# Kernel tuning notes

Hardware: AMD Instinct MI355X
Metric: run time of the kernel (lower is better)

## Reference

```python
import jax, jax.numpy as jnp
import numpy as np

DEGREE = 64
LEN_H = 2
INIT_H = 4.0
FEATURES = [256, 512, 512, 256]
BATCH = 1024


def _frozen_kh():
    # get_frozen_para: k = arange(-floor(d/2), ceil(d/2)+1); h = 1/(init_h*(1+arange(len_h))) (inverse decay)
    k = jnp.arange(-np.floor(DEGREE / 2), np.ceil(DEGREE / 2) + 1, dtype=jnp.float32)  # (degree+1,)
    h = 1.0 / (INIT_H * (1.0 + jnp.arange(LEN_H, dtype=jnp.float32)))  # (len_h,)
    return k, h


def setup_inputs() -> dict:
    key = jax.random.key(0)
    ks = jax.random.split(key, 7)
    inp = {"x": jax.random.normal(ks[0], (BATCH, FEATURES[0]), dtype=jnp.float32)}
    i = 1
    for li, (fi, fo) in enumerate(zip(FEATURES[:-1], FEATURES[1:])):
        # initialization='None': plain normal coeffs (matches source)
        inp[f"coeffs{li}"] = jax.random.normal(ks[i], (fi, fo, LEN_H, DEGREE + 1), dtype=jnp.float32)
        inp[f"alpha{li}"] = jax.random.normal(ks[i + 1], (fi, fo), dtype=jnp.float32) / jnp.sqrt((fi + fo) / 2.0)
        inp[f"beta{li}"] = jnp.zeros((fo,), dtype=jnp.float32)
        i += 2
    return inp


def _sinc_layer(x, coeffs, alpha, beta, k, h):
    # x: (b, i); coeffs: (i, o, k_h, d+1); alpha: (i, o); beta: (o,)
    y_eqt = x @ alpha + beta  # skip connection (skip_mode=1)
    xa = jnp.tanh(x)  # activation='tanh'
    # tile across (len_h, degree+1), scale by 1/h, shift by k, then sinc
    xe = xa[:, :, None, None] / h[None, None, :, None] + k[None, None, None, :]  # (b, i, k_h, d+1)
    y = jnp.einsum("bikd,iokd->bo", jnp.sinc(xe), coeffs)
    return y_eqt + y


def reference(x, coeffs0, alpha0, beta0, coeffs1, alpha1, beta1, coeffs2, alpha2, beta2):
    k, h = _frozen_kh()
    x = jnp.tanh(x)  # normalizer
    for c, a, b in ((coeffs0, alpha0, beta0), (coeffs1, alpha1, beta1), (coeffs2, alpha2, beta2)):
        x = _sinc_layer(x, c, a, b, k, h)
    return x
```

## Files before the change

kernel.cpp:

```cpp
#include <hip/hip_runtime.h>
#include <hip/hip_bf16.h>
#include <cstdint>


#define PI_F 3.14159265358979323846f

typedef float floatx4 __attribute__((ext_vector_type(4)));
typedef __bf16 bf16x8 __attribute__((ext_vector_type(8)));

#define GLOAD_LDS16(gp, lp)                                                    \
  __builtin_amdgcn_global_load_lds(                                            \
      (const __attribute__((address_space(1))) void*)(uintptr_t)(const void*)(gp), \
      (__attribute__((address_space(3))) void*)(uint32_t)(uintptr_t)(void*)(lp),   \
      16, 0, 0)

static __device__ __forceinline__ void repack_body(
    const float* __restrict__ coeffs, const float* __restrict__ alpha,
    ushort* __restrict__ Bhi, ushort* __restrict__ Blo,
    int fo, int Kaug, int writeLo, int idx, int tid)
{
  int nchunksK = Kaug >> 8;
  int o     = idx / nchunksK;
  int chunk = idx - o * nchunksK;
  int r = chunk * 256 + tid;
  int i = r / 131;
  int j = r - i * 131;
  float v;
  if (j == 130) {
    v = alpha[(size_t)i * fo + o];
  } else {
    int h1 = (j >= 65) ? 1 : 0;
    int d  = j - (h1 ? 65 : 0);
    v = coeffs[(((size_t)i * fo + o) * 2 + h1) * 65 + d];
  }
  __hip_bfloat16 hb = __float2bfloat16(v);
  Bhi[(size_t)o * Kaug + r] = *(ushort*)&hb;
  if (writeLo) {
    __hip_bfloat16 lb = __float2bfloat16(v - __bfloat162float(hb));
    Blo[(size_t)o * Kaug + r] = *(ushort*)&lb;
  }
}

__global__ __launch_bounds__(256) void repack_all(
    const float* c0, const float* a0, ushort* h0, ushort* l0,
    const float* c1, const float* a1, ushort* h1, ushort* l1,
    const float* c2, const float* a2, ushort* h2,
    int fo0, int fo1, int fo2, int K0, int K1, int K2, int nb0, int nb01)
{
  int b = blockIdx.x, tid = threadIdx.x;
  if (b < nb0)        repack_body(c0, a0, h0, l0, fo0, K0, 1, b,        tid);
  else if (b < nb01)  repack_body(c1, a1, h1, l1, fo1, K1, 1, b - nb0,  tid);
  else                repack_body(c2, a2, h2, 0,  fo2, K2, 0, b - nb01, tid);
}

__global__ __launch_bounds__(256) void repack_kernel(
    const float* __restrict__ coeffs, const float* __restrict__ alpha,
    ushort* __restrict__ Bhi, ushort* __restrict__ Blo,
    int fo, int Kaug, int writeLo)
{
  repack_body(coeffs, alpha, Bhi, Blo, fo, Kaug, writeLo,
              blockIdx.x + blockIdx.y * gridDim.x, threadIdx.x);
}

__global__ __launch_bounds__(256) void act_kernel(
    const float* __restrict__ Xin, __hip_bfloat16* __restrict__ Ahi,
    __hip_bfloat16* __restrict__ Alo, int first, int writeLo)
{
  __shared__ float sm[256][5];
  int tid = threadIdx.x;
  int p0  = blockIdx.x * 256;
  {
    float x  = Xin[p0 + tid];
    float t  = first ? tanhf(x) : x;
    float xa = tanhf(t);
    float z0 = 4.0f * xa, z1 = 8.0f * xa;
    float n0 = rintf(z0), n1 = rintf(z1);
    float s0 = sinf(PI_F * (z0 - n0)) * (1.0f / PI_F);
    float s1 = sinf(PI_F * (z1 - n1)) * (1.0f / PI_F);
    if (((int)n0) & 1) s0 = -s0;
    if (((int)n1) & 1) s1 = -s1;
    sm[tid][0] = t;
    sm[tid][1] = z0;
    sm[tid][2] = s0;
    sm[tid][3] = z1;
    sm[tid][4] = s1;
  }
  __syncthreads();
  size_t base = (size_t)p0 * 131;
  for (int e = tid; e < 256 * 131; e += 256) {
    int li = e / 131;
    int j  = e - li * 131;
    float t = sm[li][0];
    bool h1 = (j >= 65);
    int d   = h1 ? (j - 65) : j;
    float z = h1 ? sm[li][3] : sm[li][1];
    float s = h1 ? sm[li][4] : sm[li][2];
    int kk  = d - 32;
    float den = z + (float)kk;
    float v = s / den;
    if (kk & 1) v = -v;
    if (den == 0.0f) v = 1.0f;
    if (j == 130)    v = t;
    __hip_bfloat16 hb = __float2bfloat16(v);
    Ahi[base + e] = hb;
    if (writeLo)
      Alo[base + e] = __float2bfloat16(v - __bfloat162float(hb));
  }
}

__global__ __launch_bounds__(256, 4) void gemm_bf16_splitk(
    const __hip_bfloat16* __restrict__ Ahi, const __hip_bfloat16* __restrict__ Alo,
    const __hip_bfloat16* __restrict__ Bhi, const __hip_bfloat16* __restrict__ Blo,
    float* __restrict__ Cpart,
    int N, int Kaug, int totalSteps, int splitk, int tilesN, int MBN, int nterms)
{
  __shared__ __align__(16) ushort As[128 * 64];
  __shared__ __align__(16) ushort Bs[128 * 64];

  int bx    = blockIdx.x;
  int split = bx % splitk;
  int tile  = bx / splitk;
  int tm = tile / tilesN;
  int tn = tile - tm * tilesN;
  int S  = nterms * totalSteps;
  int s0 = (int)(((long long)split * S) / splitk);
  int s1 = (int)(((long long)(split + 1) * S) / splitk);

  int tid  = threadIdx.x;
  int lane = tid & 63;
  int wave = tid >> 6;
  int wm = (wave >> 1) * 64;
  int wn = (wave & 1) * 64;

  floatx4 acc[4][4];
#pragma unroll
  for (int i = 0; i < 4; i++)
#pragma unroll
    for (int j = 0; j < 4; j++) acc[i][j] = floatx4{0.f, 0.f, 0.f, 0.f};

  for (int term = 0; term < nterms; ++term) {
    int base = term * totalSteps;
    int t0 = s0 - base; if (t0 < 0) t0 = 0;
    int t1 = s1 - base; if (t1 > totalSteps) t1 = totalSteps;
    if (t0 >= t1) continue;

    const ushort* Ag = (const ushort*)((term == 1) ? Alo : Ahi)
                       + (size_t)tm * 128 * Kaug;
    const ushort* Bg = (const ushort*)((term == 2) ? Blo : Bhi)
                       + (size_t)tn * 128 * Kaug;

    for (int s = t0; s < t1; ++s) {
      int k0 = s * 64;
#pragma unroll
      for (int r = 0; r < 4; ++r) {
        int c   = tid + 256 * r;
        int row = c >> 3;
        int kcg = (c & 7) ^ (row & 7);
        GLOAD_LDS16(Ag + (size_t)row * Kaug + k0 + kcg * 8, &As[c * 8]);
      }
#pragma unroll
      for (int r = 0; r < 4; ++r) {
        int c   = tid + 256 * r;
        int row = c >> 3;
        int kcg = (c & 7) ^ (row & 7);
        GLOAD_LDS16(Bg + (size_t)row * Kaug + k0 + kcg * 8, &Bs[c * 8]);
      }
      __syncthreads();

#pragma unroll
      for (int q = 0; q < 2; ++q) {
        bf16x8 af[4], bf[4];
        int rsub = lane & 15;
        int qc   = q * 4 + (lane >> 4);
#pragma unroll
        for (int t = 0; t < 4; ++t) {
          int row = wm + t * 16 + rsub;
          af[t] = *(const bf16x8*)&As[(row * 8 + (qc ^ (row & 7))) * 8];
        }
#pragma unroll
        for (int t = 0; t < 4; ++t) {
          int row = wn + t * 16 + rsub;
          bf[t] = *(const bf16x8*)&Bs[(row * 8 + (qc ^ (row & 7))) * 8];
        }
#pragma unroll
        for (int i = 0; i < 4; ++i)
#pragma unroll
          for (int j = 0; j < 4; ++j)
            acc[i][j] = __builtin_amdgcn_mfma_f32_16x16x32_bf16(
                af[i], bf[j], acc[i][j], 0, 0, 0);
      }
      __syncthreads();
    }
  }

  float* Cp = Cpart + (size_t)split * MBN;
  int mrow0 = tm * 128 + wm + (lane >> 4) * 4;
  int ncol  = tn * 128 + wn + (lane & 15);
#pragma unroll
  for (int i = 0; i < 4; ++i) {
#pragma unroll
    for (int r = 0; r < 4; ++r) {
      int m = mrow0 + i * 16 + r;
      float* dst = Cp + (size_t)m * N + ncol;
#pragma unroll
      for (int j = 0; j < 4; ++j) dst[j * 16] = acc[i][j][r];
    }
  }
}

__global__ __launch_bounds__(256) void reduce_f32_kernel(
    const float4* __restrict__ Cp, const float* __restrict__ beta,
    float* __restrict__ Xout, int MN4, int N4mask, int splits)
{
  int e = blockIdx.x * 256 + threadIdx.x;
  if (e >= MN4) return;
  float4 sum = Cp[e];
  for (int s = 1; s < splits; ++s) {
    float4 v = Cp[(size_t)s * MN4 + e];
    sum.x += v.x; sum.y += v.y; sum.z += v.z; sum.w += v.w;
  }
  int n0 = (e & N4mask) * 4;
  sum.x += beta[n0]; sum.y += beta[n0 + 1];
  sum.z += beta[n0 + 2]; sum.w += beta[n0 + 3];
  ((float4*)Xout)[e] = sum;
}

extern "C" void kernel_launch(void* const* d_in, const int* in_sizes, int n_in,
                              void* d_out, int out_size, void* d_ws, size_t ws_size,
                              hipStream_t stream)
{
  const float* x = (const float*)d_in[0];
  const float* coeffs[3] = {(const float*)d_in[1], (const float*)d_in[4], (const float*)d_in[7]};
  const float* alpha[3]  = {(const float*)d_in[2], (const float*)d_in[5], (const float*)d_in[8]};
  const float* beta[3]   = {(const float*)d_in[3], (const float*)d_in[6], (const float*)d_in[9]};

  const int fis[3] = {256, 512, 512};
  const int fos[3] = {512, 512, 256};
  const int trm[3] = {3, 3, 1};

  const size_t KMAX = 67072;
  const size_t bsz[3] = {2ull * 512 * 33536 * 2, 2ull * 512 * 67072 * 2,
                         1ull * 256 * 67072 * 2};
  const size_t Ball   = bsz[0] + bsz[1] + bsz[2];
  const size_t B1     = 2ull * 512 * KMAX * 2;
  const size_t needX  = 2ull * 1024 * 512 * 4;

  int MB = 1024, allB = 0;
  size_t cbytes = 67108864;
  for (;;) {
    size_t aB = (size_t)MB * KMAX * 4;
    if (aB + Ball + needX + 67108864 <= ws_size) { allB = 1; cbytes = 67108864; break; }
    if (aB + B1 + needX + 67108864 <= ws_size)   { allB = 0; cbytes = 67108864; break; }
    if (aB + B1 + needX + 33554432 <= ws_size)   { allB = 0; cbytes = 33554432; break; }
    if (MB == 128) { allB = 0; cbytes = 33554432; break; }
    MB >>= 1;
  }
  int nchunks = 1024 / MB;

  char* ws = (char*)d_ws;
  __hip_bfloat16* Ahi = (__hip_bfloat16*)ws;
  __hip_bfloat16* Alo = Ahi + (size_t)MB * KMAX;
  char* Bbase = ws + (size_t)MB * KMAX * 4;
  ushort* Bh[3]; ushort* Bl[3];
  if (allB) {
    char* p = Bbase;
    for (int l = 0; l < 3; ++l) {
      Bh[l] = (ushort*)p;
      Bl[l] = (trm[l] > 1) ? (ushort*)(p + bsz[l] / 2) : 0;
      p += bsz[l];
    }
  } else {
    for (int l = 0; l < 3; ++l) {
      Bh[l] = (ushort*)Bbase;
      Bl[l] = (trm[l] > 1) ? (ushort*)(Bbase + B1 / 2) : 0;
    }
  }
  size_t bTot = allB ? Ball : B1;
  float* X1    = (float*)(Bbase + bTot);
  float* X2    = X1 + 1024 * 512;
  float* Cpart = X2 + 1024 * 512;

  if (allB) {
    int nb0 = (33536 / 256) * 512;
    int nb1 = (67072 / 256) * 512;
    int nb2 = (67072 / 256) * 256;
    repack_all<<<nb0 + nb1 + nb2, 256, 0, stream>>>(
        coeffs[0], alpha[0], Bh[0], Bl[0],
        coeffs[1], alpha[1], Bh[1], Bl[1],
        coeffs[2], alpha[2], Bh[2],
        fos[0], fos[1], fos[2], 33536, 67072, 67072, nb0, nb0 + nb1);
  }

  const float* Xl = x;
  for (int l = 0; l < 3; ++l) {
    int fi = fis[l], fo = fos[l];
    int Kaug = fi * 131;
    int totalSteps = Kaug / 64;
    int tilesN = fo / 128;
    int sk = (int)(cbytes / 4 / ((size_t)MB * fo));
    if (sk < 1) sk = 1;
    int nterms = trm[l];

    if (!allB) {
      repack_kernel<<<dim3(Kaug / 256, fo), 256, 0, stream>>>(
          coeffs[l], alpha[l], Bh[l], Bl[l], fo, Kaug, nterms > 1 ? 1 : 0);
    }

    float* Xout_f = (l == 0) ? X1 : (l == 1 ? X2 : (float*)d_out);
    for (int c = 0; c < nchunks; ++c) {
      int mb0 = c * MB;
      act_kernel<<<(MB * fi) / 256, 256, 0, stream>>>(
          Xl + (size_t)mb0 * fi, Ahi, Alo, l == 0 ? 1 : 0, nterms > 1 ? 1 : 0);
      gemm_bf16_splitk<<<(MB / 128) * tilesN * sk, 256, 0, stream>>>(
          (const __hip_bfloat16*)Ahi, (const __hip_bfloat16*)Alo,
          (const __hip_bfloat16*)Bh[l], (const __hip_bfloat16*)Bl[l],
          Cpart, fo, Kaug, totalSteps, sk, tilesN, MB * fo, nterms);
      int MN4 = MB * fo / 4;
      reduce_f32_kernel<<<(MN4 + 255) / 256, 256, 0, stream>>>(
          (const float4*)Cpart, beta[l],
          Xout_f + (size_t)mb0 * fo, MN4, fo / 4 - 1, sk);
    }
    Xl = Xout_f;
  }
}
```

Measured before the change: 1.093 ms.

## Fuse split-bf16 terms into one GEMM pass sharing hi tiles

```diff
diff --git a/kernel.cpp b/kernel.cpp
--- a/kernel.cpp
+++ b/kernel.cpp
@@ -63,8 +63,8 @@
 }
 
 __global__ __launch_bounds__(256) void act_kernel(
-    const float* __restrict__ Xin, __hip_bfloat16* __restrict__ Ahi,
-    __hip_bfloat16* __restrict__ Alo, int first, int writeLo)
+    const float* __restrict__ Xin, ushort* __restrict__ Ahi,
+    ushort* __restrict__ Alo, int first, int writeLo)
 {
   __shared__ float sm[256][5];
   int tid = threadIdx.x;
@@ -87,44 +87,53 @@
   }
   __syncthreads();
   size_t base = (size_t)p0 * 131;
-  for (int e = tid; e < 256 * 131; e += 256) {
-    int li = e / 131;
-    int j  = e - li * 131;
-    float t = sm[li][0];
-    bool h1 = (j >= 65);
-    int d   = h1 ? (j - 65) : j;
-    float z = h1 ? sm[li][3] : sm[li][1];
-    float s = h1 ? sm[li][4] : sm[li][2];
-    int kk  = d - 32;
-    float den = z + (float)kk;
-    float v = s / den;
-    if (kk & 1) v = -v;
-    if (den == 0.0f) v = 1.0f;
-    if (j == 130)    v = t;
-    __hip_bfloat16 hb = __float2bfloat16(v);
-    Ahi[base + e] = hb;
-    if (writeLo)
-      Alo[base + e] = __float2bfloat16(v - __bfloat162float(hb));
-  }
-}
-
-__global__ __launch_bounds__(256, 4) void gemm_bf16_splitk(
-    const __hip_bfloat16* __restrict__ Ahi, const __hip_bfloat16* __restrict__ Alo,
-    const __hip_bfloat16* __restrict__ Bhi, const __hip_bfloat16* __restrict__ Blo,
+  for (int e4 = tid; e4 < 64 * 131; e4 += 256) {
+    int f0 = e4 * 4;
+    ushort4 hv, lv;
+#pragma unroll
+    for (int u = 0; u < 4; ++u) {
+      int f  = f0 + u;
+      int li = f / 131;
+      int j  = f - li * 131;
+      float t = sm[li][0];
+      bool h1 = (j >= 65);
+      int d   = h1 ? (j - 65) : j;
+      float z = h1 ? sm[li][3] : sm[li][1];
+      float s = h1 ? sm[li][4] : sm[li][2];
+      int kk  = d - 32;
+      float den = z + (float)kk;
+      float v = __fdividef(s, den);
+      if (kk & 1) v = -v;
+      if (den == 0.0f) v = 1.0f;
+      if (j == 130)    v = t;
+      __hip_bfloat16 hb = __float2bfloat16(v);
+      __hip_bfloat16 lb = __float2bfloat16(v - __bfloat162float(hb));
+      ((ushort*)&hv)[u] = *(ushort*)&hb;
+      ((ushort*)&lv)[u] = *(ushort*)&lb;
+    }
+    *(ushort4*)(Ahi + base + f0) = hv;
+    if (writeLo) *(ushort4*)(Alo + base + f0) = lv;
+  }
+}
+
+__global__ __launch_bounds__(256, 4) void gemm_bf16_onepass(
+    const ushort* __restrict__ Ahi, const ushort* __restrict__ Alo,
+    const ushort* __restrict__ Bhi, const ushort* __restrict__ Blo,
     float* __restrict__ Cpart,
-    int N, int Kaug, int totalSteps, int splitk, int tilesN, int MBN, int nterms)
-{
-  __shared__ __align__(16) ushort As[128 * 64];
-  __shared__ __align__(16) ushort Bs[128 * 64];
+    int N, int Kaug, int T, int splitk, int tilesN, int MBN, int nterms)
+{
+  __shared__ __align__(16) ushort AsH[128 * 32];
+  __shared__ __align__(16) ushort AsL[128 * 32];
+  __shared__ __align__(16) ushort BsH[128 * 32];
+  __shared__ __align__(16) ushort BsL[128 * 32];
 
   int bx    = blockIdx.x;
   int split = bx % splitk;
   int tile  = bx / splitk;
   int tm = tile / tilesN;
   int tn = tile - tm * tilesN;
-  int S  = nterms * totalSteps;
-  int s0 = (int)(((long long)split * S) / splitk);
-  int s1 = (int)(((long long)(split + 1) * S) / splitk);
+  int s0 = (int)(((long long)split * T) / splitk);
+  int s1 = (int)(((long long)(split + 1) * T) / splitk);
 
   int tid  = threadIdx.x;
   int lane = tid & 63;
@@ -138,59 +147,73 @@
 #pragma unroll
     for (int j = 0; j < 4; j++) acc[i][j] = floatx4{0.f, 0.f, 0.f, 0.f};
 
-  for (int term = 0; term < nterms; ++term) {
-    int base = term * totalSteps;
-    int t0 = s0 - base; if (t0 < 0) t0 = 0;
-    int t1 = s1 - base; if (t1 > totalSteps) t1 = totalSteps;
-    if (t0 >= t1) continue;
-
-    const ushort* Ag = (const ushort*)((term == 1) ? Alo : Ahi)
-                       + (size_t)tm * 128 * Kaug;
-    const ushort* Bg = (const ushort*)((term == 2) ? Blo : Bhi)
-                       + (size_t)tn * 128 * Kaug;
-
-    for (int s = t0; s < t1; ++s) {
-      int k0 = s * 64;
-#pragma unroll
-      for (int r = 0; r < 4; ++r) {
-        int c   = tid + 256 * r;
-        int row = c >> 3;
-        int kcg = (c & 7) ^ (row & 7);
-        GLOAD_LDS16(Ag + (size_t)row * Kaug + k0 + kcg * 8, &As[c * 8]);
+  const ushort* AgH = Ahi + (size_t)tm * 128 * Kaug;
+  const ushort* AgL = Alo + (size_t)tm * 128 * Kaug;
+  const ushort* BgH = Bhi + (size_t)tn * 128 * Kaug;
+  const ushort* BgL = Blo + (size_t)tn * 128 * Kaug;
+
+  int rsub = lane & 15;
+  int qc   = lane >> 4;
+  int aoff[4], boff[4];
+#pragma unroll
+  for (int t = 0; t < 4; ++t) {
+    int ra = wm + t * 16 + rsub;
+    aoff[t] = (ra * 4 + (qc ^ (ra & 3) ^ ((ra >> 2) & 3))) * 8;
+    int rb = wn + t * 16 + rsub;
+    boff[t] = (rb * 4 + (qc ^ (rb & 3) ^ ((rb >> 2) & 3))) * 8;
+  }
+
+  for (int s = s0; s < s1; ++s) {
+    int k0 = s * 32;
+#pragma unroll
+    for (int r = 0; r < 2; ++r) {
+      int c   = tid + 256 * r;
+      int row = c >> 2;
+      int cc  = c & 3;
+      int kcg = cc ^ (row & 3) ^ ((row >> 2) & 3);
+      size_t goff = (size_t)row * Kaug + k0 + kcg * 8;
+      GLOAD_LDS16(AgH + goff, &AsH[c * 8]);
+      GLOAD_LDS16(BgH + goff, &BsH[c * 8]);
+      if (nterms > 1) {
+        GLOAD_LDS16(AgL + goff, &AsL[c * 8]);
+        GLOAD_LDS16(BgL + goff, &BsL[c * 8]);
       }
-#pragma unroll
-      for (int r = 0; r < 4; ++r) {
-        int c   = tid + 256 * r;
-        int row = c >> 3;
-        int kcg = (c & 7) ^ (row & 7);
-        GLOAD_LDS16(Bg + (size_t)row * Kaug + k0 + kcg * 8, &Bs[c * 8]);
-      }
-      __syncthreads();
-
-#pragma unroll
-      for (int q = 0; q < 2; ++q) {
-        bf16x8 af[4], bf[4];
-        int rsub = lane & 15;
-        int qc   = q * 4 + (lane >> 4);
-#pragma unroll
-        for (int t = 0; t < 4; ++t) {
-          int row = wm + t * 16 + rsub;
-          af[t] = *(const bf16x8*)&As[(row * 8 + (qc ^ (row & 7))) * 8];
-        }
-#pragma unroll
-        for (int t = 0; t < 4; ++t) {
-          int row = wn + t * 16 + rsub;
-          bf[t] = *(const bf16x8*)&Bs[(row * 8 + (qc ^ (row & 7))) * 8];
-        }
-#pragma unroll
-        for (int i = 0; i < 4; ++i)
-#pragma unroll
-          for (int j = 0; j < 4; ++j)
-            acc[i][j] = __builtin_amdgcn_mfma_f32_16x16x32_bf16(
-                af[i], bf[j], acc[i][j], 0, 0, 0);
-      }
-      __syncthreads();
-    }
+    }
+    __syncthreads();
+
+    bf16x8 ah[4], bh[4];
+#pragma unroll
+    for (int t = 0; t < 4; ++t) ah[t] = *(const bf16x8*)&AsH[aoff[t]];
+#pragma unroll
+    for (int t = 0; t < 4; ++t) bh[t] = *(const bf16x8*)&BsH[boff[t]];
+#pragma unroll
+    for (int i = 0; i < 4; ++i)
+#pragma unroll
+      for (int j = 0; j < 4; ++j)
+        acc[i][j] = __builtin_amdgcn_mfma_f32_16x16x32_bf16(
+            ah[i], bh[j], acc[i][j], 0, 0, 0);
+
+    if (nterms > 1) {
+      bf16x8 bl[4];
+#pragma unroll
+      for (int t = 0; t < 4; ++t) bl[t] = *(const bf16x8*)&BsL[boff[t]];
+#pragma unroll
+      for (int i = 0; i < 4; ++i)
+#pragma unroll
+        for (int j = 0; j < 4; ++j)
+          acc[i][j] = __builtin_amdgcn_mfma_f32_16x16x32_bf16(
+              ah[i], bl[j], acc[i][j], 0, 0, 0);
+      bf16x8 al[4];
+#pragma unroll
+      for (int t = 0; t < 4; ++t) al[t] = *(const bf16x8*)&AsL[aoff[t]];
+#pragma unroll
+      for (int i = 0; i < 4; ++i)
+#pragma unroll
+        for (int j = 0; j < 4; ++j)
+          acc[i][j] = __builtin_amdgcn_mfma_f32_16x16x32_bf16(
+              al[i], bh[j], acc[i][j], 0, 0, 0);
+    }
+    __syncthreads();
   }
 
   float* Cp = Cpart + (size_t)split * MBN;
@@ -258,21 +281,21 @@
   int nchunks = 1024 / MB;
 
   char* ws = (char*)d_ws;
-  __hip_bfloat16* Ahi = (__hip_bfloat16*)ws;
-  __hip_bfloat16* Alo = Ahi + (size_t)MB * KMAX;
+  ushort* Ahi = (ushort*)ws;
+  ushort* Alo = Ahi + (size_t)MB * KMAX;
   char* Bbase = ws + (size_t)MB * KMAX * 4;
   ushort* Bh[3]; ushort* Bl[3];
   if (allB) {
     char* p = Bbase;
     for (int l = 0; l < 3; ++l) {
       Bh[l] = (ushort*)p;
-      Bl[l] = (trm[l] > 1) ? (ushort*)(p + bsz[l] / 2) : 0;
+      Bl[l] = (trm[l] > 1) ? (ushort*)(p + bsz[l] / 2) : (ushort*)p;
       p += bsz[l];
     }
   } else {
     for (int l = 0; l < 3; ++l) {
       Bh[l] = (ushort*)Bbase;
-      Bl[l] = (trm[l] > 1) ? (ushort*)(Bbase + B1 / 2) : 0;
+      Bl[l] = (trm[l] > 1) ? (ushort*)(Bbase + B1 / 2) : (ushort*)Bbase;
     }
   }
   size_t bTot = allB ? Ball : B1;
@@ -295,7 +318,7 @@
   for (int l = 0; l < 3; ++l) {
     int fi = fis[l], fo = fos[l];
     int Kaug = fi * 131;
-    int totalSteps = Kaug / 64;
+    int T = Kaug / 32;
     int tilesN = fo / 128;
     int sk = (int)(cbytes / 4 / ((size_t)MB * fo));
     if (sk < 1) sk = 1;
@@ -311,10 +334,9 @@
       int mb0 = c * MB;
       act_kernel<<<(MB * fi) / 256, 256, 0, stream>>>(
           Xl + (size_t)mb0 * fi, Ahi, Alo, l == 0 ? 1 : 0, nterms > 1 ? 1 : 0);
-      gemm_bf16_splitk<<<(MB / 128) * tilesN * sk, 256, 0, stream>>>(
-          (const __hip_bfloat16*)Ahi, (const __hip_bfloat16*)Alo,
-          (const __hip_bfloat16*)Bh[l], (const __hip_bfloat16*)Bl[l],
-          Cpart, fo, Kaug, totalSteps, sk, tilesN, MB * fo, nterms);
+      gemm_bf16_onepass<<<(MB / 128) * tilesN * sk, 256, 0, stream>>>(
+          Ahi, (nterms > 1) ? Alo : Ahi, Bh[l], Bl[l],
+          Cpart, fo, Kaug, T, sk, tilesN, MB * fo, nterms);
       int MN4 = MB * fo / 4;
       reduce_f32_kernel<<<(MN4 + 255) / 256, 256, 0, stream>>>(
           (const float4*)Cpart, beta[l],
```

New measurement: 1.073 ms. About the same (-1.8%).
